# Performance work log

Measured on AMD Instinct MI355X. Metric: run time of the kernel, lower is better.

## Reference

```python
import jax, jax.numpy as jnp
import numpy as np

B, C, H, W = 4, 64, 64, 64
C8 = C // 8

def setup_inputs() -> dict:
    key = jax.random.key(0)
    ks = jax.random.split(key, 7)
    s = 0.05
    x  = jax.random.normal(ks[0], (B, C, H, W), dtype=jnp.float32)
    wq = jax.random.normal(ks[1], (C8, C), dtype=jnp.float32) * s
    bq = jax.random.normal(ks[2], (C8,), dtype=jnp.float32) * s
    wk = jax.random.normal(ks[3], (C8, C), dtype=jnp.float32) * s
    bk = jax.random.normal(ks[4], (C8,), dtype=jnp.float32) * s
    wv = jax.random.normal(ks[5], (C, C), dtype=jnp.float32) * s
    bv = jax.random.normal(ks[6], (C,), dtype=jnp.float32) * s
    return {"x": x, "wq": wq, "bq": bq, "wk": wk, "bk": bk, "wv": wv, "bv": bv}

def reference(x, wq, bq, wk, bk, wv, bv):
    b, c, h, w = x.shape
    n = h * w
    xf = x.reshape(b, c, n)                                   # [B,C,N]
    q = jnp.einsum('oc,bcn->bon', wq, xf) + bq[None, :, None]  # [B,C8,N]
    k = jnp.einsum('oc,bcn->bon', wk, xf) + bk[None, :, None]  # [B,C8,N]
    v = jnp.einsum('oc,bcn->bon', wv, xf) + bv[None, :, None]  # [B,C, N]
    scores = jnp.einsum('bci,bcj->bij', q, k)                  # [B,N,N]
    attn = jax.nn.softmax(scores, axis=-1)
    out = jnp.einsum('bcn,bnm->bcm', v, attn)                  # V @ A, as torch.bmm(value, attention)
    return out.reshape(b, c, h, w) + x
```

## Files before the change

kernel.cpp:

```cpp
#include <hip/hip_runtime.h>
#include <hip/hip_bf16.h>
#include <math.h>

#define NN 4096
#define CC 64

typedef float  f32x16 __attribute__((ext_vector_type(16)));
typedef short  bf16x8 __attribute__((ext_vector_type(8)));
typedef short  s16x4  __attribute__((ext_vector_type(4)));
typedef unsigned int u32x4 __attribute__((ext_vector_type(4)));

static __device__ __forceinline__ unsigned short f2bfu(float f) {
    __hip_bfloat16 h = __float2bfloat16(f);
    unsigned short s;
    __builtin_memcpy(&s, &h, 2);
    return s;
}
static __device__ __forceinline__ unsigned packbf(float lo, float hi) {
    return (unsigned)f2bfu(lo) | ((unsigned)f2bfu(hi) << 16);
}
static __device__ __forceinline__ f32x16 fzero16() {
    f32x16 z;
#pragma unroll
    for (int i = 0; i < 16; ++i) z[i] = 0.f;
    return z;
}
static __device__ __forceinline__ bf16x8 bzero8() {
    bf16x8 z;
#pragma unroll
    for (int i = 0; i < 8; ++i) z[i] = 0;
    return z;
}

__global__ __launch_bounds__(256) void proj_all(
        const float* __restrict__ x,
        const float* __restrict__ wq, const float* __restrict__ bq,
        const float* __restrict__ wk, const float* __restrict__ bk,
        const float* __restrict__ wv, const float* __restrict__ bv,
        short* __restrict__ qb, short* __restrict__ kb, float* __restrict__ vT) {
    int t = threadIdx.x;
    int w = t >> 6, ml = t & 31, hi = (t >> 5) & 1;
    int rt = blockIdx.x >> 7;
    int nt = (blockIdx.x & 127) * 4 + w;
    int ng = nt * 32 + ml;
    int b = ng >> 12, nb_ = ng & 4095;
    const float* xc = x + ((size_t)b * CC) * NN + nb_;

    int rg = 32 * rt + ml;
    const float* wrow =
        rg < 8  ? wq + (size_t)rg * 64 :
        rg < 16 ? wk + (size_t)(rg - 8) * 64 :
        rg < 80 ? wv + (size_t)(rg - 16) * 64 : wq;
    bool wvalid = (rg < 80);

    f32x16 acc = fzero16();
#pragma unroll
    for (int s = 0; s < 4; ++s) {
        int c0 = 16 * s + 8 * hi;
        float xv[8];
#pragma unroll
        for (int j = 0; j < 8; ++j) xv[j] = xc[(size_t)(c0 + j) * NN];
        u32x4 xg;
#pragma unroll
        for (int j = 0; j < 4; ++j) xg[j] = packbf(xv[2 * j], xv[2 * j + 1]);
        bf16x8 xf = __builtin_bit_cast(bf16x8, xg);

        bf16x8 af;
        if (wvalid) {
            float4 f0 = *(const float4*)(wrow + c0);
            float4 f1 = *(const float4*)(wrow + c0 + 4);
            u32x4 ag;
            ag[0] = packbf(f0.x, f0.y); ag[1] = packbf(f0.z, f0.w);
            ag[2] = packbf(f1.x, f1.y); ag[3] = packbf(f1.z, f1.w);
            af = __builtin_bit_cast(bf16x8, ag);
        } else {
            af = bzero8();
        }
        acc = __builtin_amdgcn_mfma_f32_32x32x16_bf16(af, xf, acc, 0, 0, 0);
    }

    if (rt == 0) {
        s16x4 qv, kv;
#pragma unroll
        for (int j = 0; j < 4; ++j) {
            qv[j] = (short)f2bfu(acc[j] + bq[j + 4 * hi]);
            kv[j] = (short)f2bfu(acc[j + 4] + bk[j + 4 * hi]);
        }
        *(s16x4*)(qb + (size_t)ng * 8 + 4 * hi) = qv;
        *(s16x4*)(kb + (size_t)ng * 8 + 4 * hi) = kv;
#pragma unroll
        for (int r = 8; r < 16; ++r) {
            int rowr = (r & 3) + 8 * (r >> 2) + 4 * hi;
            int c = rowr - 16;
            vT[((size_t)(b * CC + c)) * NN + nb_] = acc[r] + bv[c];
        }
    } else if (rt == 1) {
#pragma unroll
        for (int r = 0; r < 16; ++r) {
            int rowr = (r & 3) + 8 * (r >> 2) + 4 * hi;
            int c = rowr + 16;
            vT[((size_t)(b * CC + c)) * NN + nb_] = acc[r] + bv[c];
        }
    } else {
#pragma unroll
        for (int r = 0; r < 8; ++r) {
            int rowr = (r & 3) + 8 * (r >> 2) + 4 * hi;
            int c = rowr + 48;
            vT[((size_t)(b * CC + c)) * NN + nb_] = acc[r] + bv[c];
        }
    }
}

__global__ __launch_bounds__(512) void stats_mfma(
        const short* __restrict__ qb, const short* __restrict__ kb,
        float* __restrict__ rinv) {
    int b = blockIdx.x >> 7;
    int nbase = (blockIdx.x & 127) * 32;
    int t = threadIdx.x;
    int w = __builtin_amdgcn_readfirstlane(t >> 6);
    int ml = t & 31, hi = (t >> 5) & 1;

    bf16x8 qf = bzero8();
    if (!hi) qf = *(const bf16x8*)(qb + ((size_t)(b * NN + nbase + ml)) * 8);
    const short* kbb = kb + ((size_t)b * NN) * 8;

    float accl[16];
#pragma unroll
    for (int r = 0; r < 16; ++r) accl[r] = 0.f;

    bf16x8 kf0 = bzero8();
    if (!hi) kf0 = *(const bf16x8*)(kbb + (size_t)(w * 32 + ml) * 8);

    for (int i = 0; i < 16; ++i) {
        int mchn = (i < 15) ? (w + 8 * (i + 1)) : w;
        bf16x8 kf1 = bzero8();
        if (!hi) kf1 = *(const bf16x8*)(kbb + (size_t)(mchn * 32 + ml) * 8);
        f32x16 s = __builtin_amdgcn_mfma_f32_32x32x16_bf16(qf, kf0, fzero16(), 0, 0, 0);
#pragma unroll
        for (int r = 0; r < 16; ++r) accl[r] += __expf(s[r]);
        kf0 = kf1;
    }

#pragma unroll
    for (int r = 0; r < 16; ++r) {
#pragma unroll
        for (int mask = 1; mask <= 16; mask <<= 1)
            accl[r] += __shfl_xor(accl[r], mask);
    }

    __shared__ float rs[32];
    if (t < 32) rs[t] = 0.f;
    __syncthreads();
    if (ml == 0) {
#pragma unroll
        for (int r = 0; r < 16; ++r) {
            int rowr = (r & 3) + 8 * (r >> 2) + 4 * hi;
            atomicAdd(&rs[rowr], accl[r]);
        }
    }
    __syncthreads();
    if (t < 32) rinv[(size_t)b * NN + nbase + t] = 1.0f / rs[t];
}

__global__ __launch_bounds__(256) void v_scale(
        const float* __restrict__ vT, const float* __restrict__ rinv,
        short* __restrict__ vsT) {
    int gid = blockIdx.x * 256 + threadIdx.x;
    int row = gid >> 9;
    int noff = (gid & 511) << 3;
    int b = row >> 6;
    const float* vp = vT + (size_t)row * NN + noff;
    const float* rp = rinv + (size_t)b * NN + noff;
    float4 v0 = *(const float4*)vp, v1 = *(const float4*)(vp + 4);
    float4 r0 = *(const float4*)rp, r1 = *(const float4*)(rp + 4);
    u32x4 o;
    o[0] = packbf(v0.x * r0.x, v0.y * r0.y);
    o[1] = packbf(v0.z * r0.z, v0.w * r0.w);
    o[2] = packbf(v1.x * r1.x, v1.y * r1.y);
    o[3] = packbf(v1.z * r1.z, v1.w * r1.w);
    *(u32x4*)(vsT + (size_t)row * NN + noff) = o;
}

__global__ __launch_bounds__(512, 2) void attn_pv(
        const short* __restrict__ qb, const short* __restrict__ kb,
        const short* __restrict__ vsT,
        const float* __restrict__ x, float* __restrict__ out) {
    __shared__ float red[4][64][68];

    int b = blockIdx.x >> 6;
    int mbase = (blockIdx.x & 63) << 6;
    int t = threadIdx.x;
    int w = __builtin_amdgcn_readfirstlane(t >> 6);
    int ml = t & 31, hi = (t >> 5) & 1;

    bf16x8 kf0 = bzero8(), kf1 = bzero8();
    if (!hi) {
        kf0 = *(const bf16x8*)(kb + ((size_t)(b * NN + mbase + ml)) * 8);
        kf1 = *(const bf16x8*)(kb + ((size_t)(b * NN + mbase + 32 + ml)) * 8);
    }

    f32x16 accA = fzero16(), accB = fzero16();
    f32x16 accC = fzero16(), accD = fzero16();

    const short* qbb = qb + ((size_t)b * NN) * 8;
    const short* v0p = vsT + ((size_t)(b * CC) + ml) * NN;
    const short* v1p = v0p + (size_t)32 * NN;

    int n0 = w * 32;
    bf16x8 qf_c = bzero8();
    if (!hi) qf_c = *(const bf16x8*)(qbb + (size_t)(n0 + ml) * 8);
    bf16x8 a00_c = *(const bf16x8*)(v0p + n0 + 8 * hi);
    bf16x8 a01_c = *(const bf16x8*)(v0p + n0 + 16 + 8 * hi);
    bf16x8 a10_c = *(const bf16x8*)(v1p + n0 + 8 * hi);
    bf16x8 a11_c = *(const bf16x8*)(v1p + n0 + 16 + 8 * hi);

    for (int i = 0; i < 16; ++i) {
        int n0n = (i < 15) ? (w + 8 * (i + 1)) * 32 : w * 32;
        bf16x8 qf_n = bzero8();
        if (!hi) qf_n = *(const bf16x8*)(qbb + (size_t)(n0n + ml) * 8);
        bf16x8 a00_n = *(const bf16x8*)(v0p + n0n + 8 * hi);
        bf16x8 a01_n = *(const bf16x8*)(v0p + n0n + 16 + 8 * hi);
        bf16x8 a10_n = *(const bf16x8*)(v1p + n0n + 8 * hi);
        bf16x8 a11_n = *(const bf16x8*)(v1p + n0n + 16 + 8 * hi);

        f32x16 s0 = __builtin_amdgcn_mfma_f32_32x32x16_bf16(qf_c, kf0, fzero16(), 0, 0, 0);
        f32x16 s1 = __builtin_amdgcn_mfma_f32_32x32x16_bf16(qf_c, kf1, fzero16(), 0, 0, 0);

        unsigned g0 = packbf(__expf(s0[0]),  __expf(s0[1]));
        unsigned g1 = packbf(__expf(s0[2]),  __expf(s0[3]));
        unsigned g2 = packbf(__expf(s0[4]),  __expf(s0[5]));
        unsigned g3 = packbf(__expf(s0[6]),  __expf(s0[7]));
        unsigned g4 = packbf(__expf(s0[8]),  __expf(s0[9]));
        unsigned g5 = packbf(__expf(s0[10]), __expf(s0[11]));
        unsigned g6 = packbf(__expf(s0[12]), __expf(s0[13]));
        unsigned g7 = packbf(__expf(s0[14]), __expf(s0[15]));
        unsigned gr0 = (unsigned)__shfl_xor((int)(hi ? g0 : g2), 32);
        unsigned gr1 = (unsigned)__shfl_xor((int)(hi ? g1 : g3), 32);
        unsigned gr2 = (unsigned)__shfl_xor((int)(hi ? g4 : g6), 32);
        unsigned gr3 = (unsigned)__shfl_xor((int)(hi ? g5 : g7), 32);
        u32x4 b0u, b1u;
        b0u[0] = hi ? gr0 : g0;  b0u[1] = hi ? gr1 : g1;
        b0u[2] = hi ? g2 : gr0;  b0u[3] = hi ? g3 : gr1;
        b1u[0] = hi ? gr2 : g4;  b1u[1] = hi ? gr3 : g5;
        b1u[2] = hi ? g6 : gr2;  b1u[3] = hi ? g7 : gr3;
        bf16x8 bf00 = __builtin_bit_cast(bf16x8, b0u);
        bf16x8 bf01 = __builtin_bit_cast(bf16x8, b1u);

        unsigned h0 = packbf(__expf(s1[0]),  __expf(s1[1]));
        unsigned h1 = packbf(__expf(s1[2]),  __expf(s1[3]));
        unsigned h2 = packbf(__expf(s1[4]),  __expf(s1[5]));
        unsigned h3 = packbf(__expf(s1[6]),  __expf(s1[7]));
        unsigned h4 = packbf(__expf(s1[8]),  __expf(s1[9]));
        unsigned h5 = packbf(__expf(s1[10]), __expf(s1[11]));
        unsigned h6 = packbf(__expf(s1[12]), __expf(s1[13]));
        unsigned h7 = packbf(__expf(s1[14]), __expf(s1[15]));
        unsigned hr0 = (unsigned)__shfl_xor((int)(hi ? h0 : h2), 32);
        unsigned hr1 = (unsigned)__shfl_xor((int)(hi ? h1 : h3), 32);
        unsigned hr2 = (unsigned)__shfl_xor((int)(hi ? h4 : h6), 32);
        unsigned hr3 = (unsigned)__shfl_xor((int)(hi ? h5 : h7), 32);
        u32x4 b2u, b3u;
        b2u[0] = hi ? hr0 : h0;  b2u[1] = hi ? hr1 : h1;
        b2u[2] = hi ? h2 : hr0;  b2u[3] = hi ? h3 : hr1;
        b3u[0] = hi ? hr2 : h4;  b3u[1] = hi ? hr3 : h5;
        b3u[2] = hi ? h6 : hr2;  b3u[3] = hi ? h7 : hr3;
        bf16x8 bf10 = __builtin_bit_cast(bf16x8, b2u);
        bf16x8 bf11 = __builtin_bit_cast(bf16x8, b3u);

        accA = __builtin_amdgcn_mfma_f32_32x32x16_bf16(a00_c, bf00, accA, 0, 0, 0);
        accA = __builtin_amdgcn_mfma_f32_32x32x16_bf16(a01_c, bf01, accA, 0, 0, 0);
        accC = __builtin_amdgcn_mfma_f32_32x32x16_bf16(a10_c, bf00, accC, 0, 0, 0);
        accC = __builtin_amdgcn_mfma_f32_32x32x16_bf16(a11_c, bf01, accC, 0, 0, 0);
        accB = __builtin_amdgcn_mfma_f32_32x32x16_bf16(a00_c, bf10, accB, 0, 0, 0);
        accB = __builtin_amdgcn_mfma_f32_32x32x16_bf16(a01_c, bf11, accB, 0, 0, 0);
        accD = __builtin_amdgcn_mfma_f32_32x32x16_bf16(a10_c, bf10, accD, 0, 0, 0);
        accD = __builtin_amdgcn_mfma_f32_32x32x16_bf16(a11_c, bf11, accD, 0, 0, 0);

        qf_c = qf_n;
        a00_c = a00_n; a01_c = a01_n; a10_c = a10_n; a11_c = a11_n;
    }

    int q4 = w & 3;
    if (w >= 4) {
#pragma unroll
        for (int r = 0; r < 16; ++r) {
            int rowr = (r & 3) + 8 * (r >> 2) + 4 * hi;
            red[q4][rowr][ml]           = accA[r];
            red[q4][rowr][32 + ml]      = accB[r];
            red[q4][rowr + 32][ml]      = accC[r];
            red[q4][rowr + 32][32 + ml] = accD[r];
        }
    }
    __syncthreads();
    if (w < 4) {
#pragma unroll
        for (int r = 0; r < 16; ++r) {
            int rowr = (r & 3) + 8 * (r >> 2) + 4 * hi;
            red[q4][rowr][ml]           += accA[r];
            red[q4][rowr][32 + ml]      += accB[r];
            red[q4][rowr + 32][ml]      += accC[r];
            red[q4][rowr + 32][32 + ml] += accD[r];
        }
    }
    __syncthreads();

    int c = t >> 3;
    int m0 = (t & 7) << 3;
    float4 s0 = *(float4*)&red[0][c][m0];
    float4 s1 = *(float4*)&red[0][c][m0 + 4];
#pragma unroll
    for (int q = 1; q < 4; ++q) {
        float4 a = *(float4*)&red[q][c][m0];
        float4 b4 = *(float4*)&red[q][c][m0 + 4];
        s0.x += a.x; s0.y += a.y; s0.z += a.z; s0.w += a.w;
        s1.x += b4.x; s1.y += b4.y; s1.z += b4.z; s1.w += b4.w;
    }
    size_t idx = ((size_t)(b * CC + c)) * NN + mbase + m0;
    float4 xa = *(const float4*)(x + idx);
    float4 xb = *(const float4*)(x + idx + 4);
    s0.x += xa.x; s0.y += xa.y; s0.z += xa.z; s0.w += xa.w;
    s1.x += xb.x; s1.y += xb.y; s1.z += xb.z; s1.w += xb.w;
    *(float4*)(out + idx) = s0;
    *(float4*)(out + idx + 4) = s1;
}

extern "C" void kernel_launch(void* const* d_in, const int* in_sizes, int n_in,
                              void* d_out, int out_size, void* d_ws, size_t ws_size,
                              hipStream_t stream) {
    const float* x  = (const float*)d_in[0];
    const float* wq = (const float*)d_in[1];
    const float* bq = (const float*)d_in[2];
    const float* wk = (const float*)d_in[3];
    const float* bk = (const float*)d_in[4];
    const float* wv = (const float*)d_in[5];
    const float* bv = (const float*)d_in[6];
    float* out = (float*)d_out;

    char* ws = (char*)d_ws;
    short* qb   = (short*)(ws);
    short* kb   = (short*)(ws + (256u << 10));
    float* vT   = (float*)(ws + (512u << 10));
    short* vsT  = (short*)(ws + (512u << 10) + (4u << 20));
    float* rinv = (float*)(ws + (512u << 10) + (6u << 20));

    proj_all  <<<384, 256, 0, stream>>>(x, wq, bq, wk, bk, wv, bv, qb, kb, vT);
    stats_mfma<<<512, 512, 0, stream>>>(qb, kb, rinv);
    v_scale   <<<512, 256, 0, stream>>>(vT, rinv, vsT);
    attn_pv   <<<256, 512, 0, stream>>>(qb, kb, vsT, x, out);
}
```

Measured before the change: 48.33 us.

## Fuse softmax normalization into attention loop and use exp2 with pre-scaled Q

Result: slower. 49.95 us (+3.4%).

```diff
diff --git a/kernel.cpp b/kernel.cpp
--- a/kernel.cpp
+++ b/kernel.cpp
@@ -4,6 +4,7 @@
 
 #define NN 4096
 #define CC 64
+#define LOG2E 1.44269504f
 
 typedef float  f32x16 __attribute__((ext_vector_type(16)));
 typedef short  bf16x8 __attribute__((ext_vector_type(8)));
@@ -19,6 +20,11 @@
 static __device__ __forceinline__ unsigned packbf(float lo, float hi) {
     return (unsigned)f2bfu(lo) | ((unsigned)f2bfu(hi) << 16);
 }
+static __device__ __forceinline__ float exp2_fast(float x) {
+    float r;
+    asm("v_exp_f32 %0, %1" : "=v"(r) : "v"(x));
+    return r;
+}
 static __device__ __forceinline__ f32x16 fzero16() {
     f32x16 z;
 #pragma unroll
@@ -37,7 +43,7 @@
         const float* __restrict__ wq, const float* __restrict__ bq,
         const float* __restrict__ wk, const float* __restrict__ bk,
         const float* __restrict__ wv, const float* __restrict__ bv,
-        short* __restrict__ qb, short* __restrict__ kb, float* __restrict__ vT) {
+        short* __restrict__ qb, short* __restrict__ kb, short* __restrict__ vsT) {
     int t = threadIdx.x;
     int w = t >> 6, ml = t & 31, hi = (t >> 5) & 1;
     int rt = blockIdx.x >> 7;
@@ -83,7 +89,7 @@
         s16x4 qv, kv;
 #pragma unroll
         for (int j = 0; j < 4; ++j) {
-            qv[j] = (short)f2bfu(acc[j] + bq[j + 4 * hi]);
+            qv[j] = (short)f2bfu((acc[j] + bq[j + 4 * hi]) * LOG2E);
             kv[j] = (short)f2bfu(acc[j + 4] + bk[j + 4 * hi]);
         }
         *(s16x4*)(qb + (size_t)ng * 8 + 4 * hi) = qv;
@@ -92,21 +98,21 @@
         for (int r = 8; r < 16; ++r) {
             int rowr = (r & 3) + 8 * (r >> 2) + 4 * hi;
             int c = rowr - 16;
-            vT[((size_t)(b * CC + c)) * NN + nb_] = acc[r] + bv[c];
+            vsT[((size_t)(b * CC + c)) * NN + nb_] = (short)f2bfu(acc[r] + bv[c]);
         }
     } else if (rt == 1) {
 #pragma unroll
         for (int r = 0; r < 16; ++r) {
             int rowr = (r & 3) + 8 * (r >> 2) + 4 * hi;
             int c = rowr + 16;
-            vT[((size_t)(b * CC + c)) * NN + nb_] = acc[r] + bv[c];
+            vsT[((size_t)(b * CC + c)) * NN + nb_] = (short)f2bfu(acc[r] + bv[c]);
         }
     } else {
 #pragma unroll
         for (int r = 0; r < 8; ++r) {
             int rowr = (r & 3) + 8 * (r >> 2) + 4 * hi;
             int c = rowr + 48;
-            vT[((size_t)(b * CC + c)) * NN + nb_] = acc[r] + bv[c];
+            vsT[((size_t)(b * CC + c)) * NN + nb_] = (short)f2bfu(acc[r] + bv[c]);
         }
     }
 }
@@ -137,7 +143,7 @@
         if (!hi) kf1 = *(const bf16x8*)(kbb + (size_t)(mchn * 32 + ml) * 8);
         f32x16 s = __builtin_amdgcn_mfma_f32_32x32x16_bf16(qf, kf0, fzero16(), 0, 0, 0);
 #pragma unroll
-        for (int r = 0; r < 16; ++r) accl[r] += __expf(s[r]);
+        for (int r = 0; r < 16; ++r) accl[r] += exp2_fast(s[r]);
         kf0 = kf1;
     }
 
@@ -162,28 +168,9 @@
     if (t < 32) rinv[(size_t)b * NN + nbase + t] = 1.0f / rs[t];
 }
 
-__global__ __launch_bounds__(256) void v_scale(
-        const float* __restrict__ vT, const float* __restrict__ rinv,
-        short* __restrict__ vsT) {
-    int gid = blockIdx.x * 256 + threadIdx.x;
-    int row = gid >> 9;
-    int noff = (gid & 511) << 3;
-    int b = row >> 6;
-    const float* vp = vT + (size_t)row * NN + noff;
-    const float* rp = rinv + (size_t)b * NN + noff;
-    float4 v0 = *(const float4*)vp, v1 = *(const float4*)(vp + 4);
-    float4 r0 = *(const float4*)rp, r1 = *(const float4*)(rp + 4);
-    u32x4 o;
-    o[0] = packbf(v0.x * r0.x, v0.y * r0.y);
-    o[1] = packbf(v0.z * r0.z, v0.w * r0.w);
-    o[2] = packbf(v1.x * r1.x, v1.y * r1.y);
-    o[3] = packbf(v1.z * r1.z, v1.w * r1.w);
-    *(u32x4*)(vsT + (size_t)row * NN + noff) = o;
-}
-
 __global__ __launch_bounds__(512, 2) void attn_pv(
         const short* __restrict__ qb, const short* __restrict__ kb,
-        const short* __restrict__ vsT,
+        const short* __restrict__ vsT, const float* __restrict__ rinv,
         const float* __restrict__ x, float* __restrict__ out) {
     __shared__ float red[4][64][68];
 
@@ -205,6 +192,7 @@
     const short* qbb = qb + ((size_t)b * NN) * 8;
     const short* v0p = vsT + ((size_t)(b * CC) + ml) * NN;
     const short* v1p = v0p + (size_t)32 * NN;
+    const float* rvb = rinv + (size_t)b * NN;
 
     int n0 = w * 32;
     bf16x8 qf_c = bzero8();
@@ -213,6 +201,11 @@
     bf16x8 a01_c = *(const bf16x8*)(v0p + n0 + 16 + 8 * hi);
     bf16x8 a10_c = *(const bf16x8*)(v1p + n0 + 8 * hi);
     bf16x8 a11_c = *(const bf16x8*)(v1p + n0 + 16 + 8 * hi);
+    const float* rvp = rvb + n0 + 4 * hi;
+    float4 rv0_c = *(const float4*)(rvp);
+    float4 rv1_c = *(const float4*)(rvp + 8);
+    float4 rv2_c = *(const float4*)(rvp + 16);
+    float4 rv3_c = *(const float4*)(rvp + 24);
 
     for (int i = 0; i < 16; ++i) {
         int n0n = (i < 15) ? (w + 8 * (i + 1)) * 32 : w * 32;
@@ -222,18 +215,23 @@
         bf16x8 a01_n = *(const bf16x8*)(v0p + n0n + 16 + 8 * hi);
         bf16x8 a10_n = *(const bf16x8*)(v1p + n0n + 8 * hi);
         bf16x8 a11_n = *(const bf16x8*)(v1p + n0n + 16 + 8 * hi);
+        const float* rvpn = rvb + n0n + 4 * hi;
+        float4 rv0_n = *(const float4*)(rvpn);
+        float4 rv1_n = *(const float4*)(rvpn + 8);
+        float4 rv2_n = *(const float4*)(rvpn + 16);
+        float4 rv3_n = *(const float4*)(rvpn + 24);
 
         f32x16 s0 = __builtin_amdgcn_mfma_f32_32x32x16_bf16(qf_c, kf0, fzero16(), 0, 0, 0);
         f32x16 s1 = __builtin_amdgcn_mfma_f32_32x32x16_bf16(qf_c, kf1, fzero16(), 0, 0, 0);
 
-        unsigned g0 = packbf(__expf(s0[0]),  __expf(s0[1]));
-        unsigned g1 = packbf(__expf(s0[2]),  __expf(s0[3]));
-        unsigned g2 = packbf(__expf(s0[4]),  __expf(s0[5]));
-        unsigned g3 = packbf(__expf(s0[6]),  __expf(s0[7]));
-        unsigned g4 = packbf(__expf(s0[8]),  __expf(s0[9]));
-        unsigned g5 = packbf(__expf(s0[10]), __expf(s0[11]));
-        unsigned g6 = packbf(__expf(s0[12]), __expf(s0[13]));
-        unsigned g7 = packbf(__expf(s0[14]), __expf(s0[15]));
+        unsigned g0 = packbf(exp2_fast(s0[0])  * rv0_c.x, exp2_fast(s0[1])  * rv0_c.y);
+        unsigned g1 = packbf(exp2_fast(s0[2])  * rv0_c.z, exp2_fast(s0[3])  * rv0_c.w);
+        unsigned g2 = packbf(exp2_fast(s0[4])  * rv1_c.x, exp2_fast(s0[5])  * rv1_c.y);
+        unsigned g3 = packbf(exp2_fast(s0[6])  * rv1_c.z, exp2_fast(s0[7])  * rv1_c.w);
+        unsigned g4 = packbf(exp2_fast(s0[8])  * rv2_c.x, exp2_fast(s0[9])  * rv2_c.y);
+        unsigned g5 = packbf(exp2_fast(s0[10]) * rv2_c.z, exp2_fast(s0[11]) * rv2_c.w);
+        unsigned g6 = packbf(exp2_fast(s0[12]) * rv3_c.x, exp2_fast(s0[13]) * rv3_c.y);
+        unsigned g7 = packbf(exp2_fast(s0[14]) * rv3_c.z, exp2_fast(s0[15]) * rv3_c.w);
         unsigned gr0 = (unsigned)__shfl_xor((int)(hi ? g0 : g2), 32);
         unsigned gr1 = (unsigned)__shfl_xor((int)(hi ? g1 : g3), 32);
         unsigned gr2 = (unsigned)__shfl_xor((int)(hi ? g4 : g6), 32);
@@ -246,14 +244,14 @@
         bf16x8 bf00 = __builtin_bit_cast(bf16x8, b0u);
         bf16x8 bf01 = __builtin_bit_cast(bf16x8, b1u);
 
-        unsigned h0 = packbf(__expf(s1[0]),  __expf(s1[1]));
-        unsigned h1 = packbf(__expf(s1[2]),  __expf(s1[3]));
-        unsigned h2 = packbf(__expf(s1[4]),  __expf(s1[5]));
-        unsigned h3 = packbf(__expf(s1[6]),  __expf(s1[7]));
-        unsigned h4 = packbf(__expf(s1[8]),  __expf(s1[9]));
-        unsigned h5 = packbf(__expf(s1[10]), __expf(s1[11]));
-        unsigned h6 = packbf(__expf(s1[12]), __expf(s1[13]));
-        unsigned h7 = packbf(__expf(s1[14]), __expf(s1[15]));
+        unsigned h0 = packbf(exp2_fast(s1[0])  * rv0_c.x, exp2_fast(s1[1])  * rv0_c.y);
+        unsigned h1 = packbf(exp2_fast(s1[2])  * rv0_c.z, exp2_fast(s1[3])  * rv0_c.w);
+        unsigned h2 = packbf(exp2_fast(s1[4])  * rv1_c.x, exp2_fast(s1[5])  * rv1_c.y);
+        unsigned h3 = packbf(exp2_fast(s1[6])  * rv1_c.z, exp2_fast(s1[7])  * rv1_c.w);
+        unsigned h4 = packbf(exp2_fast(s1[8])  * rv2_c.x, exp2_fast(s1[9])  * rv2_c.y);
+        unsigned h5 = packbf(exp2_fast(s1[10]) * rv2_c.z, exp2_fast(s1[11]) * rv2_c.w);
+        unsigned h6 = packbf(exp2_fast(s1[12]) * rv3_c.x, exp2_fast(s1[13]) * rv3_c.y);
+        unsigned h7 = packbf(exp2_fast(s1[14]) * rv3_c.z, exp2_fast(s1[15]) * rv3_c.w);
         unsigned hr0 = (unsigned)__shfl_xor((int)(hi ? h0 : h2), 32);
         unsigned hr1 = (unsigned)__shfl_xor((int)(hi ? h1 : h3), 32);
         unsigned hr2 = (unsigned)__shfl_xor((int)(hi ? h4 : h6), 32);
@@ -277,6 +275,7 @@
 
         qf_c = qf_n;
         a00_c = a00_n; a01_c = a01_n; a10_c = a10_n; a11_c = a11_n;
+        rv0_c = rv0_n; rv1_c = rv1_n; rv2_c = rv2_n; rv3_c = rv3_n;
     }
 
     int q4 = w & 3;
@@ -338,12 +337,10 @@
     char* ws = (char*)d_ws;
     short* qb   = (short*)(ws);
     short* kb   = (short*)(ws + (256u << 10));
-    float* vT   = (float*)(ws + (512u << 10));
-    short* vsT  = (short*)(ws + (512u << 10) + (4u << 20));
-    float* rinv = (float*)(ws + (512u << 10) + (6u << 20));
-
-    proj_all  <<<384, 256, 0, stream>>>(x, wq, bq, wk, bk, wv, bv, qb, kb, vT);
+    short* vsT  = (short*)(ws + (512u << 10));
+    float* rinv = (float*)(ws + (512u << 10) + (2u << 20));
+
+    proj_all  <<<384, 256, 0, stream>>>(x, wq, bq, wk, bk, wv, bv, qb, kb, vsT);
     stats_mfma<<<512, 512, 0, stream>>>(qb, kb, rinv);
-    v_scale   <<<512, 256, 0, stream>>>(vT, rinv, vsT);
-    attn_pv   <<<256, 512, 0, stream>>>(qb, kb, vsT, x, out);
-}
+    attn_pv   <<<256, 512, 0, stream>>>(qb, kb, vsT, rinv, x, out);
+}
```
